# Optimization experiments

Hardware: AMD Instinct MI355X
Metric: run time of the kernel (lower is better)

Reference implementation:

```python
import jax, jax.numpy as jnp
import numpy as np

DIM = 768
H = 12
D = DIM // H            # 64
SCALE = D ** -0.5
M = 64                  # landmarks for pnp heads
PINV_ITERS = 6
PNP_HEADS = 11          # heads 0..10 use Nystrom, head 11 uses softmax


def setup_inputs() -> dict:
    key = jax.random.key(0)
    ks = jax.random.split(key, 5)
    B, N = 4, 4096
    x = jax.random.normal(ks[0], (B, N, DIM), jnp.float32)
    qkv_w = jax.random.normal(ks[1], (3 * DIM, DIM), jnp.float32) * (DIM ** -0.5)
    qkv_b = jax.random.normal(ks[2], (3 * DIM,), jnp.float32) * 0.01
    proj_w = jax.random.normal(ks[3], (DIM, DIM), jnp.float32) * (DIM ** -0.5)
    proj_b = jax.random.normal(ks[4], (DIM,), jnp.float32) * 0.01
    return {"x": x, "qkv_w": qkv_w, "qkv_b": qkv_b, "proj_w": proj_w, "proj_b": proj_b}


def moore_penrose_iter_pinv(x, iters=PINV_ITERS):
    # x: [B, h, M, M]. Original torch code takes torch.max over the whole per-head
    # tensor (incl. batch), so normalize with a per-head scalar over axes (B, M).
    abs_x = jnp.abs(x)
    col_max = abs_x.sum(axis=-1, keepdims=True).max(axis=(0, 2, 3), keepdims=True)
    row_max = abs_x.sum(axis=-2, keepdims=True).max(axis=(0, 2, 3), keepdims=True)
    z = jnp.swapaxes(x, -1, -2) / (col_max * row_max)
    I = jnp.eye(x.shape[-1], dtype=x.dtype)
    for _ in range(iters):
        xz = x @ z
        z = 0.25 * (z @ (13.0 * I - xz @ (15.0 * I - xz @ (7.0 * I - xz))))
    return z


def reference(x, qkv_w, qkv_b, proj_w, proj_b):
    B, N, C = x.shape
    qkv = (x @ qkv_w.T + qkv_b).reshape(B, N, 3, H, D).transpose(2, 0, 3, 1, 4)  # [3,B,H,N,D]
    q, k, v = qkv[0] * SCALE, qkv[1], qkv[2]

    # ---- Nystrom (pnp) heads 0..PNP_HEADS-1, all with the same M -> vectorized ----
    qp, kp, vp = q[:, :PNP_HEADS], k[:, :PNP_HEADS], v[:, :PNP_HEADS]
    idxs = jnp.array([int(i * N / M) for i in range(M)], dtype=jnp.int32)
    q_m = qp[:, :, idxs, :]   # [B,h,M,D] landmark queries
    k_m = kp[:, :, idxs, :]   # [B,h,M,D] landmark keys

    SA = jnp.einsum('bhnd,bhmd->bhnm', qp, k_m)   # [B,h,N,M]
    SC = jnp.einsum('bhmd,bhnd->bhmn', q_m, kp)   # [B,h,M,N]
    SB = jnp.einsum('bhmd,bhld->bhml', q_m, k_m)  # [B,h,M,M]

    eA = jnp.exp(SA - SA.max(axis=-1, keepdims=True))
    sc_max = SC.max(axis=-1, keepdims=True)       # [B,h,M,1]
    eC = jnp.exp(SC - sc_max)
    eB = jnp.exp(jnp.clip(SB - sc_max, -88.0, None))

    v_aug = jnp.concatenate([vp, jnp.ones_like(vp[..., :1])], axis=-1)  # [B,h,N,D+1]
    pi = moore_penrose_iter_pinv(eB)
    prod = (eA @ pi) @ (eC @ v_aug)               # [B,h,N,D+1]
    out_p = prod[..., :-1] / jnp.maximum(prod[..., -1:], 1e-8)

    # ---- fallback softmax head(s) ----
    qs, ks_, vs = q[:, PNP_HEADS:], k[:, PNP_HEADS:], v[:, PNP_HEADS:]
    attn = jax.nn.softmax(jnp.einsum('bhnd,bhmd->bhnm', qs, ks_), axis=-1)
    out_s = attn @ vs

    ctx = jnp.concatenate([out_p, out_s], axis=1).transpose(0, 2, 1, 3).reshape(B, N, C)
    return ctx @ proj_w.T + proj_b
```

## Files before the change

kernel.cpp:

```cpp
#include <hip/hip_runtime.h>


typedef __attribute__((ext_vector_type(8))) short short8;
typedef __attribute__((ext_vector_type(4))) float f32x4;
typedef __attribute__((ext_vector_type(4))) unsigned short ushort4v;

static __device__ __forceinline__ unsigned short f2bf(float f) {
    union { float f; unsigned u; } x; x.f = f;
    unsigned r = x.u + 0x7fffu + ((x.u >> 16) & 1u);
    return (unsigned short)(r >> 16);
}

static __device__ __forceinline__ float b2f(unsigned short u) {
    union { unsigned u; float f; } t; t.u = (unsigned)u << 16; return t.f;
}

static __device__ __forceinline__ void bfsplit(float x, unsigned short& h, unsigned short& l) {
    unsigned short hh = f2bf(x);
    union { unsigned u; float f; } t; t.u = (unsigned)hh << 16;
    h = hh;
    l = f2bf(x - t.f);
}

__global__ __launch_bounds__(256) void preconv3(
    const float* __restrict__ a, const float* __restrict__ b,
    const float* __restrict__ c,
    unsigned short* __restrict__ ahi, unsigned short* __restrict__ alo,
    unsigned short* __restrict__ bhi, unsigned short* __restrict__ blo,
    unsigned short* __restrict__ chi, unsigned short* __restrict__ clo)
{
    const int nA = 3145728, nB = 442368, nC = 147456;
    const int total = nA + nB + nC;
    for (int i = blockIdx.x * 256 + threadIdx.x; i < total; i += gridDim.x * 256) {
        const float* src; unsigned short* hi; unsigned short* lo; int j;
        if (i < nA)           { src = a; hi = ahi; lo = alo; j = i; }
        else if (i < nA + nB) { src = b; hi = bhi; lo = blo; j = i - nA; }
        else                  { src = c; hi = chi; lo = clo; j = i - nA - nB; }
        float4 f = *(const float4*)(src + (size_t)j * 4);
        float vs[4] = {f.x, f.y, f.z, f.w};
        ushort4v h, l;
        #pragma unroll
        for (int t = 0; t < 4; ++t) {
            unsigned short hh, ll;
            bfsplit(vs[t], hh, ll);
            h[t] = hh; l[t] = ll;
        }
        *(ushort4v*)(hi + (size_t)j * 4) = h;
        *(ushort4v*)(lo + (size_t)j * 4) = l;
    }
}

__global__ __launch_bounds__(256, 2) void gemm_qkv2(
    const unsigned short* __restrict__ Xh, const unsigned short* __restrict__ Xl,
    const unsigned short* __restrict__ Wh, const unsigned short* __restrict__ Wl,
    const float* __restrict__ bias,
    unsigned short* __restrict__ qh, unsigned short* __restrict__ ql,
    unsigned short* __restrict__ kh, unsigned short* __restrict__ kl,
    unsigned short* __restrict__ vh)
{
    __shared__ unsigned short smem[16384];
    const int tid = threadIdx.x;
    const int ln = tid & 63, wv = tid >> 6;
    const int wr = (wv >> 1) << 6, wc = (wv & 1) << 6;
    const int fr = ln & 15, fc = ln >> 4;
    const int fg = ln >> 4;

    if (blockIdx.x < 1536) {
        unsigned short* Ah = smem;
        unsigned short* Al = smem + 4096;
        unsigned short* Bh = smem + 8192;
        unsigned short* Bl = smem + 12288;
        const int bid = blockIdx.x;
        const int swz = (bid & 7) * 192 + (bid >> 3);
        const int brow = (swz / 12) << 7, bcol = (swz % 12) << 7;
        const int srow = tid >> 1, sc = (tid & 1) << 1;
        const size_t ag = (size_t)(brow + srow) * 768 + (sc << 3);
        const size_t bg = (size_t)(bcol + srow) * 768 + (sc << 3);
        const int i0 = srow * 32 + (((sc + 0) ^ (srow & 3)) << 3);
        const int i1 = srow * 32 + (((sc + 1) ^ (srow & 3)) << 3);

        f32x4 acc[4][4] = {};
        for (int k0 = 0; k0 < 768; k0 += 32) {
            short8 xh0 = *(const short8*)(Xh + ag + k0);
            short8 xh1 = *(const short8*)(Xh + ag + k0 + 8);
            short8 xl0 = *(const short8*)(Xl + ag + k0);
            short8 xl1 = *(const short8*)(Xl + ag + k0 + 8);
            short8 wh0 = *(const short8*)(Wh + bg + k0);
            short8 wh1 = *(const short8*)(Wh + bg + k0 + 8);
            short8 wl0 = *(const short8*)(Wl + bg + k0);
            short8 wl1 = *(const short8*)(Wl + bg + k0 + 8);
            __syncthreads();
            *(short8*)&Ah[i0] = xh0; *(short8*)&Ah[i1] = xh1;
            *(short8*)&Al[i0] = xl0; *(short8*)&Al[i1] = xl1;
            *(short8*)&Bh[i0] = wh0; *(short8*)&Bh[i1] = wh1;
            *(short8*)&Bl[i0] = wl0; *(short8*)&Bl[i1] = wl1;
            __syncthreads();
            short8 ah[4], al[4], bh[4], bl[4];
            #pragma unroll
            for (int i = 0; i < 4; ++i) {
                int ar = wr + (i << 4) + fr;
                int aidx = ar * 32 + ((fc ^ (ar & 3)) << 3);
                ah[i] = *(short8*)&Ah[aidx];
                al[i] = *(short8*)&Al[aidx];
                int br2 = wc + (i << 4) + fr;
                int bidx = br2 * 32 + ((fc ^ (br2 & 3)) << 3);
                bh[i] = *(short8*)&Bh[bidx];
                bl[i] = *(short8*)&Bl[bidx];
            }
            #pragma unroll
            for (int i = 0; i < 4; ++i)
                #pragma unroll
                for (int j = 0; j < 4; ++j) {
                    acc[i][j] = __builtin_amdgcn_mfma_f32_16x16x32_bf16(ah[i], bh[j], acc[i][j], 0, 0, 0);
                    acc[i][j] = __builtin_amdgcn_mfma_f32_16x16x32_bf16(ah[i], bl[j], acc[i][j], 0, 0, 0);
                    acc[i][j] = __builtin_amdgcn_mfma_f32_16x16x32_bf16(al[i], bh[j], acc[i][j], 0, 0, 0);
                }
        }
        #pragma unroll
        for (int j = 0; j < 4; ++j) {
            int c = bcol + wc + (j << 4) + fr;
            float bb = bias[c];
            int rem = c - (c >= 768 ? 768 : 0);
            int h = rem >> 6, d = rem & 63;
            #pragma unroll
            for (int i = 0; i < 4; ++i)
                #pragma unroll
                for (int r = 0; r < 4; ++r) {
                    int row = brow + wr + (i << 4) + (fg << 2) + r;
                    int b = row >> 12, n = row & 4095;
                    float val = acc[i][j][r] + bb;
                    size_t idx = (((size_t)(b * 12 + h) << 12) + n) * 64 + d;
                    unsigned short hh, ll;
                    if (c < 768) {
                        bfsplit(val * 0.125f, hh, ll);
                        qh[idx] = hh; ql[idx] = ll;
                    } else {
                        bfsplit(val, hh, ll);
                        kh[idx] = hh; kl[idx] = ll;
                    }
                }
        }
    } else {
        unsigned short* Av = smem;
        unsigned short* Bv = smem + 8192;
        const int bid = blockIdx.x - 1536;
        const int swz = (bid & 7) * 96 + (bid >> 3);
        const int brow = (swz / 6) << 7, bcol = 1536 + ((swz % 6) << 7);
        const int srow = tid >> 1;
        const int c0 = (tid & 1) << 2;
        const size_t ag = (size_t)(brow + srow) * 768;
        const size_t bg = (size_t)(bcol + srow) * 768;

        f32x4 acc[4][4] = {};
        for (int k0 = 0; k0 < 768; k0 += 64) {
            short8 xa[4], wb[4];
            #pragma unroll
            for (int cc = 0; cc < 4; ++cc) {
                xa[cc] = *(const short8*)(Xh + ag + k0 + ((c0 + cc) << 3));
                wb[cc] = *(const short8*)(Wh + bg + k0 + ((c0 + cc) << 3));
            }
            __syncthreads();
            #pragma unroll
            for (int cc = 0; cc < 4; ++cc) {
                int dst = srow * 64 + (((c0 + cc) ^ (srow & 7)) << 3);
                *(short8*)&Av[dst] = xa[cc];
                *(short8*)&Bv[dst] = wb[cc];
            }
            __syncthreads();
            #pragma unroll
            for (int ks = 0; ks < 2; ++ks) {
                const int kc = (ks << 2) + fc;
                short8 ah[4], bh[4];
                #pragma unroll
                for (int i = 0; i < 4; ++i) {
                    int ar = wr + (i << 4) + fr;
                    ah[i] = *(short8*)&Av[ar * 64 + ((kc ^ (ar & 7)) << 3)];
                    int br2 = wc + (i << 4) + fr;
                    bh[i] = *(short8*)&Bv[br2 * 64 + ((kc ^ (br2 & 7)) << 3)];
                }
                #pragma unroll
                for (int i = 0; i < 4; ++i)
                    #pragma unroll
                    for (int j = 0; j < 4; ++j)
                        acc[i][j] = __builtin_amdgcn_mfma_f32_16x16x32_bf16(ah[i], bh[j], acc[i][j], 0, 0, 0);
            }
        }
        #pragma unroll
        for (int j = 0; j < 4; ++j) {
            int c = bcol + wc + (j << 4) + fr;
            float bb = bias[c];
            int rem = c - 1536;
            int h = rem >> 6, d = rem & 63;
            #pragma unroll
            for (int i = 0; i < 4; ++i)
                #pragma unroll
                for (int r = 0; r < 4; ++r) {
                    int row = brow + wr + (i << 4) + (fg << 2) + r;
                    int b = row >> 12, n = row & 4095;
                    float val = acc[i][j][r] + bb;
                    size_t idx = (((size_t)(b * 12 + h) << 12) + n) * 64 + d;
                    vh[idx] = f2bf(val);
                }
        }
    }
}

__global__ __launch_bounds__(256) void attn_mega(
    const unsigned short* __restrict__ qh, const unsigned short* __restrict__ ql,
    const unsigned short* __restrict__ khg, const unsigned short* __restrict__ klg,
    const unsigned short* __restrict__ vhg,
    float* __restrict__ wacc, float* __restrict__ wl, float* __restrict__ wm,
    float* __restrict__ pacc, float* __restrict__ pm, float* __restrict__ pl)
{
    __shared__ unsigned short kh_s[64][72], kl_s[64][72];
    __shared__ unsigned short vth[64][72];
    __shared__ unsigned short ph[4][16][72];
    int tid = threadIdx.x;
    int wv = tid >> 6, ln = tid & 63;
    int rr = tid >> 2, dg = (tid & 3) << 4;
    const int arow = (wv << 4) + (ln & 15);
    const int ak0 = (ln >> 4) << 3;
    const int rg = (ln >> 4) << 2;

    if (blockIdx.x < 1024) {
        int fbid = blockIdx.x;
        int bx = fbid & 63, cy = (fbid >> 6) & 3, b = fbid >> 8;
        int n0 = bx << 6;
        size_t base = ((size_t)(b * 12 + 11)) << 12;
        {
            size_t off = ((base + n0 + rr) << 6) + dg;
            *(short8*)&kh_s[rr][dg]     = *(const short8*)(qh + off);
            *(short8*)&kh_s[rr][dg + 8] = *(const short8*)(qh + off + 8);
        }
        __syncthreads();
        short8 aq0 = *(short8*)&kh_s[arow][ak0];
        short8 aq1 = *(short8*)&kh_s[arow][ak0 + 32];
        f32x4 o_acc[4] = {};
        float mr[4] = {-1e30f, -1e30f, -1e30f, -1e30f};
        float lr[4] = {};
        for (int t = 0; t < 16; ++t) {
            int m0 = (cy << 10) + (t << 6);
            __syncthreads();
            {
                size_t off = ((base + m0 + rr) << 6) + dg;
                *(short8*)&kl_s[rr][dg]     = *(const short8*)(khg + off);
                *(short8*)&kl_s[rr][dg + 8] = *(const short8*)(khg + off + 8);
                short8 v0 = *(const short8*)(vhg + off);
                short8 v1 = *(const short8*)(vhg + off + 8);
                #pragma unroll
                for (int i = 0; i < 8; ++i) {
                    vth[dg + i][rr]     = (unsigned short)v0[i];
                    vth[dg + 8 + i][rr] = (unsigned short)v1[i];
                }
            }
            __syncthreads();
            f32x4 s_acc[4];
            #pragma unroll
            for (int jb = 0; jb < 4; ++jb) {
                f32x4 z = {};
                short8 bk0 = *(short8*)&kl_s[(jb << 4) + (ln & 15)][ak0];
                short8 bk1 = *(short8*)&kl_s[(jb << 4) + (ln & 15)][ak0 + 32];
                z = __builtin_amdgcn_mfma_f32_16x16x32_bf16(aq0, bk0, z, 0, 0, 0);
                z = __builtin_amdgcn_mfma_f32_16x16x32_bf16(aq1, bk1, z, 0, 0, 0);
                s_acc[jb] = z;
            }
            float mx[4];
            #pragma unroll
            for (int r = 0; r < 4; ++r)
                mx[r] = fmaxf(fmaxf(s_acc[0][r], s_acc[1][r]),
                              fmaxf(s_acc[2][r], s_acc[3][r]));
            #pragma unroll
            for (int off2 = 1; off2 < 16; off2 <<= 1)
                #pragma unroll
                for (int r = 0; r < 4; ++r)
                    mx[r] = fmaxf(mx[r], __shfl_xor(mx[r], off2, 64));
            float fac[4];
            #pragma unroll
            for (int r = 0; r < 4; ++r) {
                float mn = fmaxf(mr[r], mx[r]);
                fac[r] = expf(mr[r] - mn);
                mr[r] = mn;
            }
            float rs[4] = {};
            #pragma unroll
            for (int jb = 0; jb < 4; ++jb)
                #pragma unroll
                for (int r = 0; r < 4; ++r) {
                    float p = expf(s_acc[jb][r] - mr[r]);
                    rs[r] += p;
                    ph[wv][rg + r][(jb << 4) + (ln & 15)] = f2bf(p);
                }
            #pragma unroll
            for (int off2 = 1; off2 < 16; off2 <<= 1)
                #pragma unroll
                for (int r = 0; r < 4; ++r)
                    rs[r] += __shfl_xor(rs[r], off2, 64);
            #pragma unroll
            for (int r = 0; r < 4; ++r) lr[r] = lr[r] * fac[r] + rs[r];
            #pragma unroll
            for (int jb = 0; jb < 4; ++jb)
                #pragma unroll
                for (int r = 0; r < 4; ++r)
                    o_acc[jb][r] *= fac[r];
            short8 pa0 = *(short8*)&ph[wv][ln & 15][ak0];
            short8 pa1 = *(short8*)&ph[wv][ln & 15][ak0 + 32];
            #pragma unroll
            for (int jb = 0; jb < 4; ++jb) {
                short8 bv0 = *(short8*)&vth[(jb << 4) + (ln & 15)][ak0];
                short8 bv1 = *(short8*)&vth[(jb << 4) + (ln & 15)][ak0 + 32];
                f32x4 z = o_acc[jb];
                z = __builtin_amdgcn_mfma_f32_16x16x32_bf16(pa0, bv0, z, 0, 0, 0);
                z = __builtin_amdgcn_mfma_f32_16x16x32_bf16(pa1, bv1, z, 0, 0, 0);
                o_acc[jb] = z;
            }
        }
        int slot = (b * 4 + cy) * 64 + bx;
        #pragma unroll
        for (int jb = 0; jb < 4; ++jb)
            #pragma unroll
            for (int r = 0; r < 4; ++r) {
                int row = (wv << 4) + rg + r, col = (jb << 4) + (ln & 15);
                pacc[(size_t)slot * 4096 + (size_t)row * 64 + col] = o_acc[jb][r];
            }
        if ((ln & 15) == 0)
            #pragma unroll
            for (int r = 0; r < 4; ++r) {
                int row = (wv << 4) + rg + r;
                pm[(size_t)slot * 64 + row] = mr[r];
                pl[(size_t)slot * 64 + row] = lr[r];
            }
    } else {
        int wbid = blockIdx.x - 1024;
        int chunk = wbid & 7;
        int bh = wbid >> 3;
        int b = bh / 11, h = bh - b * 11;
        size_t base = ((size_t)(b * 12 + h)) << 12;
        short8 aqh0, aql0, aqh1, aql1;
        {
            size_t off = ((base + ((size_t)arow << 6)) << 6) + ak0;
            aqh0 = *(const short8*)(qh + off);
            aqh1 = *(const short8*)(qh + off + 32);
            aql0 = *(const short8*)(ql + off);
            aql1 = *(const short8*)(ql + off + 32);
        }
        f32x4 o_acc[4] = {};
        float mr[4] = {-1e30f, -1e30f, -1e30f, -1e30f};
        float lr[4] = {};
        for (int t = 0; t < 8; ++t) {
            int n0 = (chunk << 9) + (t << 6);
            __syncthreads();
            {
                size_t off = ((base + n0 + rr) << 6) + dg;
                *(short8*)&kh_s[rr][dg]     = *(const short8*)(khg + off);
                *(short8*)&kh_s[rr][dg + 8] = *(const short8*)(khg + off + 8);
                *(short8*)&kl_s[rr][dg]     = *(const short8*)(klg + off);
                *(short8*)&kl_s[rr][dg + 8] = *(const short8*)(klg + off + 8);
                short8 v0 = *(const short8*)(vhg + off);
                short8 v1 = *(const short8*)(vhg + off + 8);
                #pragma unroll
                for (int i = 0; i < 8; ++i) {
                    vth[dg + i][rr]     = (unsigned short)v0[i];
                    vth[dg + 8 + i][rr] = (unsigned short)v1[i];
                }
            }
            __syncthreads();
            f32x4 s_acc[4];
            #pragma unroll
            for (int jb = 0; jb < 4; ++jb) {
                f32x4 z = {};
                const int brow2 = (jb << 4) + (ln & 15);
                short8 bh0 = *(short8*)&kh_s[brow2][ak0];
                short8 bh1 = *(short8*)&kh_s[brow2][ak0 + 32];
                short8 bl0 = *(short8*)&kl_s[brow2][ak0];
                short8 bl1 = *(short8*)&kl_s[brow2][ak0 + 32];
                z = __builtin_amdgcn_mfma_f32_16x16x32_bf16(aqh0, bh0, z, 0, 0, 0);
                z = __builtin_amdgcn_mfma_f32_16x16x32_bf16(aqh0, bl0, z, 0, 0, 0);
                z = __builtin_amdgcn_mfma_f32_16x16x32_bf16(aql0, bh0, z, 0, 0, 0);
                z = __builtin_amdgcn_mfma_f32_16x16x32_bf16(aqh1, bh1, z, 0, 0, 0);
                z = __builtin_amdgcn_mfma_f32_16x16x32_bf16(aqh1, bl1, z, 0, 0, 0);
                z = __builtin_amdgcn_mfma_f32_16x16x32_bf16(aql1, bh1, z, 0, 0, 0);
                s_acc[jb] = z;
            }
            float mx[4];
            #pragma unroll
            for (int r = 0; r < 4; ++r)
                mx[r] = fmaxf(fmaxf(s_acc[0][r], s_acc[1][r]),
                              fmaxf(s_acc[2][r], s_acc[3][r]));
            #pragma unroll
            for (int off2 = 1; off2 < 16; off2 <<= 1)
                #pragma unroll
                for (int r = 0; r < 4; ++r)
                    mx[r] = fmaxf(mx[r], __shfl_xor(mx[r], off2, 64));
            float fac[4];
            #pragma unroll
            for (int r = 0; r < 4; ++r) {
                float mn = fmaxf(mr[r], mx[r]);
                fac[r] = expf(mr[r] - mn);
                mr[r] = mn;
            }
            float rs[4] = {};
            #pragma unroll
            for (int jb = 0; jb < 4; ++jb)
                #pragma unroll
                for (int r = 0; r < 4; ++r) {
                    float p = expf(s_acc[jb][r] - mr[r]);
                    rs[r] += p;
                    ph[wv][rg + r][(jb << 4) + (ln & 15)] = f2bf(p);
                }
            #pragma unroll
            for (int off2 = 1; off2 < 16; off2 <<= 1)
                #pragma unroll
                for (int r = 0; r < 4; ++r)
                    rs[r] += __shfl_xor(rs[r], off2, 64);
            #pragma unroll
            for (int r = 0; r < 4; ++r) lr[r] = lr[r] * fac[r] + rs[r];
            #pragma unroll
            for (int jb = 0; jb < 4; ++jb)
                #pragma unroll
                for (int r = 0; r < 4; ++r)
                    o_acc[jb][r] *= fac[r];
            short8 pah0 = *(short8*)&ph[wv][ln & 15][ak0];
            short8 pah1 = *(short8*)&ph[wv][ln & 15][ak0 + 32];
            #pragma unroll
            for (int jb = 0; jb < 4; ++jb) {
                const int brow2 = (jb << 4) + (ln & 15);
                short8 bv0 = *(short8*)&vth[brow2][ak0];
                short8 bv1 = *(short8*)&vth[brow2][ak0 + 32];
                f32x4 o = o_acc[jb];
                o = __builtin_amdgcn_mfma_f32_16x16x32_bf16(pah0, bv0, o, 0, 0, 0);
                o = __builtin_amdgcn_mfma_f32_16x16x32_bf16(pah1, bv1, o, 0, 0, 0);
                o_acc[jb] = o;
            }
        }
        int cidx = (bh << 3) + chunk;
        #pragma unroll
        for (int jb = 0; jb < 4; ++jb)
            #pragma unroll
            for (int r = 0; r < 4; ++r) {
                int row = (wv << 4) + rg + r, col = (jb << 4) + (ln & 15);
                wacc[((size_t)cidx << 12) + ((size_t)row << 6) + col] = o_acc[jb][r];
            }
        if ((ln & 15) == 0)
            #pragma unroll
            for (int r = 0; r < 4; ++r) {
                int row = (wv << 4) + rg + r;
                wl[cidx * 64 + row] = lr[r];
                wm[cidx * 64 + row] = mr[r];
            }
    }
}

__global__ __launch_bounds__(256) void wmerge_eb(
    const float* __restrict__ wacc, const float* __restrict__ wl,
    const float* __restrict__ wm,
    const unsigned short* __restrict__ qh, const unsigned short* __restrict__ ql,
    const unsigned short* __restrict__ kh, const unsigned short* __restrict__ kl,
    float* __restrict__ Wb, float* __restrict__ eB)
{
    int bh = blockIdx.x;
    int b = bh / 11, h = bh - b * 11;
    size_t base = ((size_t)(b * 12 + h)) << 12;
    int tid = threadIdx.x;
    __shared__ float fcs[8][64];
    __shared__ float scms[64];
    __shared__ float qm[64][65], km[64][65];
    for (int e = tid; e < 4096; e += 256) {
        int mm = e >> 6, d = e & 63;
        size_t off = ((base + ((size_t)mm << 6)) << 6) + d;
        qm[mm][d] = b2f(qh[off]) + b2f(ql[off]);
        km[mm][d] = b2f(kh[off]) + b2f(kl[off]);
    }
    if (tid < 64) {
        float mx = -1e30f;
        #pragma unroll
        for (int c = 0; c < 8; ++c)
            mx = fmaxf(mx, wm[((bh << 3) + c) * 64 + tid]);
        scms[tid] = mx;
        #pragma unroll
        for (int c = 0; c < 8; ++c)
            fcs[c][tid] = expf(wm[((bh << 3) + c) * 64 + tid] - mx);
    }
    __syncthreads();
    for (int e = tid; e < 4096; e += 256) {
        int m = e >> 6, j = e & 63;
        float s = 0.f;
        #pragma unroll
        for (int c = 0; c < 8; ++c)
            s += fcs[c][m] * wacc[((size_t)((bh << 3) + c) << 12) + e];
        Wb[(size_t)bh * 4160 + m * 65 + j] = s;
    }
    if (tid < 64) {
        float s = 0.f;
        #pragma unroll
        for (int c = 0; c < 8; ++c)
            s += fcs[c][tid] * wl[((bh << 3) + c) * 64 + tid];
        Wb[(size_t)bh * 4160 + tid * 65 + 64] = s;
    }
    int m = tid >> 2, l0 = tid & 3;
    float smax = scms[m];
    for (int l = l0; l < 64; l += 4) {
        float s = 0.f;
        #pragma unroll
        for (int d = 0; d < 64; ++d) s += qm[m][d] * km[l][d];
        eB[((size_t)bh << 12) + (m << 6) + l] = expf(fmaxf(s - smax, -88.f));
    }
}

__global__ __launch_bounds__(256) void norms_kernel(
    const float* __restrict__ eB, float* __restrict__ denom)
{
    int h = blockIdx.x;
    int tid = threadIdx.x;
    int b = tid >> 6, idx = tid & 63;
    int bh = b * 11 + h;
    const float* E = eB + ((size_t)bh << 12);
    float rs = 0.f, cs = 0.f;
    #pragma unroll 4
    for (int l = 0; l < 64; ++l) rs += E[(idx << 6) + l];
    #pragma unroll 4
    for (int m = 0; m < 64; ++m) cs += E[(m << 6) + idx];
    __shared__ float r1[256], r2[256];
    r1[tid] = rs; r2[tid] = cs;
    __syncthreads();
    for (int s = 128; s > 0; s >>= 1) {
        if (tid < s) {
            r1[tid] = fmaxf(r1[tid], r1[tid + s]);
            r2[tid] = fmaxf(r2[tid], r2[tid + s]);
        }
        __syncthreads();
    }
    if (tid == 0) denom[h] = r1[0] * r2[0];
}

__device__ __forceinline__ void mm64x3(
    const unsigned short (&Ahi)[64][72], const unsigned short (&Alo)[64][72],
    const unsigned short (&BThi)[64][72], const unsigned short (&BTlo)[64][72],
    int wr, int wc, int fr, int fk, f32x4 (&acc)[2][2])
{
    #pragma unroll
    for (int ks = 0; ks < 2; ++ks) {
        const int kb = (ks << 5) + fk;
        short8 ah[2], al[2], bh[2], bl[2];
        #pragma unroll
        for (int i = 0; i < 2; ++i) {
            ah[i] = *(const short8*)&Ahi[wr + (i << 4) + fr][kb];
            al[i] = *(const short8*)&Alo[wr + (i << 4) + fr][kb];
            bh[i] = *(const short8*)&BThi[wc + (i << 4) + fr][kb];
            bl[i] = *(const short8*)&BTlo[wc + (i << 4) + fr][kb];
        }
        #pragma unroll
        for (int i = 0; i < 2; ++i)
            #pragma unroll
            for (int j = 0; j < 2; ++j) {
                acc[i][j] = __builtin_amdgcn_mfma_f32_16x16x32_bf16(ah[i], bh[j], acc[i][j], 0, 0, 0);
                acc[i][j] = __builtin_amdgcn_mfma_f32_16x16x32_bf16(ah[i], bl[j], acc[i][j], 0, 0, 0);
                acc[i][j] = __builtin_amdgcn_mfma_f32_16x16x32_bf16(al[i], bh[j], acc[i][j], 0, 0, 0);
            }
    }
}

__global__ __launch_bounds__(256) void pinv_kernel(
    const float* __restrict__ eB, const float* __restrict__ denom,
    float* __restrict__ pi_)
{
    __shared__ unsigned short Xh[64][72],  Xl[64][72];
    __shared__ unsigned short Zh[64][72],  Zl[64][72];
    __shared__ unsigned short ZTh[64][72], ZTl[64][72];
    __shared__ unsigned short Mh[64][72],  Ml[64][72];
    __shared__ unsigned short MTh[64][72], MTl[64][72];
    __shared__ unsigned short Th[64][72],  Tbl[64][72];
    __shared__ float Zf[64][68];
    int bh = blockIdx.x;
    int h = bh % 11;
    int tid = threadIdx.x;
    float dn = denom[h];
    const int ln = tid & 63, wv = tid >> 6;
    const int wr = (wv >> 1) << 5, wc = (wv & 1) << 5;
    const int fr = ln & 15, fk = (ln >> 4) << 3;
    const int rg = (ln >> 4) << 2;

    for (int e = tid; e < 4096; e += 256) {
        int m = e >> 6, l = e & 63;
        float xv = eB[((size_t)bh << 12) + e];
        unsigned short hh, ll;
        bfsplit(xv, hh, ll);
        Xh[m][l] = hh; Xl[m][l] = ll;
        float zv = xv / dn;
        Zf[l][m] = zv;
        bfsplit(zv, hh, ll);
        Zh[l][m] = hh; Zl[l][m] = ll;
        ZTh[m][l] = hh; ZTl[m][l] = ll;
    }
    __syncthreads();

    for (int it = 0; it < 6; ++it) {
        f32x4 mm1[2][2] = {};
        mm64x3(Xh, Xl, ZTh, ZTl, wr, wc, fr, fk, mm1);
        #pragma unroll
        for (int i = 0; i < 2; ++i)
            #pragma unroll
            for (int j = 0; j < 2; ++j)
                #pragma unroll
                for (int r = 0; r < 4; ++r) {
                    int row = wr + (i << 4) + rg + r, col = wc + (j << 4) + fr;
                    unsigned short hh, ll;
                    bfsplit(mm1[i][j][r], hh, ll);
                    Mh[row][col] = hh;  Ml[row][col] = ll;
                    MTh[col][row] = hh; MTl[col][row] = ll;
                }
        __syncthreads();
        f32x4 a2[2][2] = {};
        mm64x3(Mh, Ml, MTh, MTl, wr, wc, fr, fk, a2);
        #pragma unroll
        for (int i = 0; i < 2; ++i)
            #pragma unroll
            for (int j = 0; j < 2; ++j)
                #pragma unroll
                for (int r = 0; r < 4; ++r) {
                    int row = wr + (i << 4) + rg + r, col = wc + (j << 4) + fr;
                    float val = 7.f * mm1[i][j][r] - a2[i][j][r];
                    unsigned short hh, ll;
                    bfsplit(val, hh, ll);
                    Th[col][row] = hh; Tbl[col][row] = ll;
                }
        __syncthreads();
        f32x4 a3[2][2] = {};
        mm64x3(Mh, Ml, Th, Tbl, wr, wc, fr, fk, a3);
        __syncthreads();
        #pragma unroll
        for (int i = 0; i < 2; ++i)
            #pragma unroll
            for (int j = 0; j < 2; ++j)
                #pragma unroll
                for (int r = 0; r < 4; ++r) {
                    int row = wr + (i << 4) + rg + r, col = wc + (j << 4) + fr;
                    float val = 15.f * mm1[i][j][r] - a3[i][j][r];
                    unsigned short hh, ll;
                    bfsplit(val, hh, ll);
                    Th[col][row] = hh; Tbl[col][row] = ll;
                }
        __syncthreads();
        f32x4 a4[2][2] = {};
        mm64x3(Zh, Zl, Th, Tbl, wr, wc, fr, fk, a4);
        float zn[2][2][4];
        #pragma unroll
        for (int i = 0; i < 2; ++i)
            #pragma unroll
            for (int j = 0; j < 2; ++j)
                #pragma unroll
                for (int r = 0; r < 4; ++r) {
                    int row = wr + (i << 4) + rg + r, col = wc + (j << 4) + fr;
                    zn[i][j][r] = 0.25f * (13.f * Zf[row][col] - a4[i][j][r]);
                }
        __syncthreads();
        #pragma unroll
        for (int i = 0; i < 2; ++i)
            #pragma unroll
            for (int j = 0; j < 2; ++j)
                #pragma unroll
                for (int r = 0; r < 4; ++r) {
                    int row = wr + (i << 4) + rg + r, col = wc + (j << 4) + fr;
                    float val = zn[i][j][r];
                    Zf[row][col] = val;
                    unsigned short hh, ll;
                    bfsplit(val, hh, ll);
                    Zh[row][col] = hh;  Zl[row][col] = ll;
                    ZTh[col][row] = hh; ZTl[col][row] = ll;
                }
        __syncthreads();
    }
    for (int e = tid; e < 4096; e += 256)
        pi_[((size_t)bh << 12) + e] = Zf[e >> 6][e & 63];
}

__global__ __launch_bounds__(256) void pw_kernel(
    const float* __restrict__ pi_, const float* __restrict__ Wb,
    float* __restrict__ Tb)
{
    int bh = blockIdx.x;
    __shared__ float P[64][65];
    __shared__ float Wl[64][66];
    int tid = threadIdx.x;
    for (int e = tid; e < 4096; e += 256)
        P[e >> 6][e & 63] = pi_[((size_t)bh << 12) + e];
    for (int e = tid; e < 64 * 65; e += 256) {
        int l = e / 65, j = e - l * 65;
        Wl[l][j] = Wb[(size_t)bh * 4160 + e];
    }
    __syncthreads();
    int m = tid & 63, g = tid >> 6;
    #pragma unroll
    for (int t = 0; t < 17; ++t) {
        int j = g + (t << 2);
        if (j > 64) break;
        float s = 0.f;
        #pragma unroll
        for (int l = 0; l < 64; ++l) s += P[m][l] * Wl[l][j];
        Tb[(size_t)((bh << 6) + m) * 65 + j] = s;
    }
}

__global__ __launch_bounds__(256) void outp_merge(
    const unsigned short* __restrict__ qh, const unsigned short* __restrict__ ql,
    const unsigned short* __restrict__ khg, const unsigned short* __restrict__ klg,
    const float* __restrict__ Tb,
    const float* __restrict__ pacc, const float* __restrict__ pm,
    const float* __restrict__ pl,
    unsigned short* __restrict__ ctxh)
{
    int tid = threadIdx.x;
    if (blockIdx.x < 2816) {
        int bh = blockIdx.x >> 6;
        int bx = blockIdx.x & 63;
        int b = bh / 11, h = bh - b * 11;
        int n0 = bx << 6;
        size_t base = ((size_t)(b * 12 + h)) << 12;
        __shared__ unsigned short kmh[64][72], kml[64][72];
        __shared__ unsigned short tth[64][72], ttl[64][72];
        __shared__ unsigned short ph[4][16][72];
        __shared__ float t64[64];
        int wv = tid >> 6, ln = tid & 63;
        int rr = tid >> 2, dg = (tid & 3) << 4;
        const int arow = (wv << 4) + (ln & 15);
        const int ak0 = (ln >> 4) << 3;
        const int rg = (ln >> 4) << 2;
        {
            size_t off = ((base + ((size_t)rr << 6)) << 6) + dg;
            *(short8*)&kmh[rr][dg]     = *(const short8*)(khg + off);
            *(short8*)&kmh[rr][dg + 8] = *(const short8*)(khg + off + 8);
            *(short8*)&kml[rr][dg]     = *(const short8*)(klg + off);
            *(short8*)&kml[rr][dg + 8] = *(const short8*)(klg + off + 8);
        }
        for (int e = tid; e < 4096; e += 256) {
            int m = e >> 6, j = e & 63;
            float tv = Tb[(size_t)((bh << 6) + m) * 65 + j];
            unsigned short hh, ll;
            bfsplit(tv, hh, ll);
            tth[j][m] = hh; ttl[j][m] = ll;
        }
        if (tid < 64) t64[tid] = Tb[(size_t)((bh << 6) + tid) * 65 + 64];
        short8 aqh0, aql0, aqh1, aql1;
        {
            size_t off = ((base + n0 + arow) << 6) + ak0;
            aqh0 = *(const short8*)(qh + off);
            aqh1 = *(const short8*)(qh + off + 32);
            aql0 = *(const short8*)(ql + off);
            aql1 = *(const short8*)(ql + off + 32);
        }
        __syncthreads();
        f32x4 s_acc[4];
        #pragma unroll
        for (int jb = 0; jb < 4; ++jb) {
            f32x4 z = {};
            const int brow2 = (jb << 4) + (ln & 15);
            short8 bh0 = *(short8*)&kmh[brow2][ak0];
            short8 bh1 = *(short8*)&kmh[brow2][ak0 + 32];
            short8 bl0 = *(short8*)&kml[brow2][ak0];
            short8 bl1 = *(short8*)&kml[brow2][ak0 + 32];
            z = __builtin_amdgcn_mfma_f32_16x16x32_bf16(aqh0, bh0, z, 0, 0, 0);
            z = __builtin_amdgcn_mfma_f32_16x16x32_bf16(aqh0, bl0, z, 0, 0, 0);
            z = __builtin_amdgcn_mfma_f32_16x16x32_bf16(aql0, bh0, z, 0, 0, 0);
            z = __builtin_amdgcn_mfma_f32_16x16x32_bf16(aqh1, bh1, z, 0, 0, 0);
            z = __builtin_amdgcn_mfma_f32_16x16x32_bf16(aqh1, bl1, z, 0, 0, 0);
            z = __builtin_amdgcn_mfma_f32_16x16x32_bf16(aql1, bh1, z, 0, 0, 0);
            s_acc[jb] = z;
        }
        float mx[4];
        #pragma unroll
        for (int r = 0; r < 4; ++r)
            mx[r] = fmaxf(fmaxf(s_acc[0][r], s_acc[1][r]),
                          fmaxf(s_acc[2][r], s_acc[3][r]));
        #pragma unroll
        for (int off2 = 1; off2 < 16; off2 <<= 1)
            #pragma unroll
            for (int r = 0; r < 4; ++r)
                mx[r] = fmaxf(mx[r], __shfl_xor(mx[r], off2, 64));
        float den[4] = {};
        #pragma unroll
        for (int jb = 0; jb < 4; ++jb) {
            float tj = t64[(jb << 4) + (ln & 15)];
            #pragma unroll
            for (int r = 0; r < 4; ++r) {
                float p = expf(s_acc[jb][r] - mx[r]);
                den[r] += p * tj;
                ph[wv][rg + r][(jb << 4) + (ln & 15)] = f2bf(p);
            }
        }
        #pragma unroll
        for (int off2 = 1; off2 < 16; off2 <<= 1)
            #pragma unroll
            for (int r = 0; r < 4; ++r)
                den[r] += __shfl_xor(den[r], off2, 64);
        short8 pah0 = *(short8*)&ph[wv][ln & 15][ak0];
        short8 pah1 = *(short8*)&ph[wv][ln & 15][ak0 + 32];
        f32x4 o_acc[4] = {};
        #pragma unroll
        for (int jb = 0; jb < 4; ++jb) {
            const int brow2 = (jb << 4) + (ln & 15);
            short8 bth0 = *(short8*)&tth[brow2][ak0];
            short8 bth1 = *(short8*)&tth[brow2][ak0 + 32];
            short8 btl0 = *(short8*)&ttl[brow2][ak0];
            short8 btl1 = *(short8*)&ttl[brow2][ak0 + 32];
            f32x4 o = o_acc[jb];
            o = __builtin_amdgcn_mfma_f32_16x16x32_bf16(pah0, bth0, o, 0, 0, 0);
            o = __builtin_amdgcn_mfma_f32_16x16x32_bf16(pah0, btl0, o, 0, 0, 0);
            o = __builtin_amdgcn_mfma_f32_16x16x32_bf16(pah1, bth1, o, 0, 0, 0);
            o = __builtin_amdgcn_mfma_f32_16x16x32_bf16(pah1, btl1, o, 0, 0, 0);
            o_acc[jb] = o;
        }
        float inv[4];
        #pragma unroll
        for (int r = 0; r < 4; ++r) inv[r] = 1.0f / fmaxf(den[r], 1e-8f);
        #pragma unroll
        for (int jb = 0; jb < 4; ++jb)
            #pragma unroll
            for (int r = 0; r < 4; ++r) {
                int row = n0 + (wv << 4) + rg + r;
                int col = (jb << 4) + (ln & 15);
                ctxh[((size_t)b * 4096 + row) * 768 + h * 64 + col] =
                    f2bf(o_acc[jb][r] * inv[r]);
            }
    } else {
        int fb = blockIdx.x - 2816;
        int bx = fb & 63, b = fb >> 6;
        int r = tid & 63, g = tid >> 6;
        float mc[4], mt = -1e30f;
        #pragma unroll
        for (int c = 0; c < 4; ++c) {
            mc[c] = pm[(size_t)((b * 4 + c) * 64 + bx) * 64 + r];
            mt = fmaxf(mt, mc[c]);
        }
        float fac[4], lt = 0.f;
        #pragma unroll
        for (int c = 0; c < 4; ++c) {
            fac[c] = expf(mc[c] - mt);
            lt += fac[c] * pl[(size_t)((b * 4 + c) * 64 + bx) * 64 + r];
        }
        float inv = 1.0f / lt;
        size_t obase = ((size_t)b * 4096 + (size_t)((bx << 6) + r)) * 768 + 11 * 64 + (g << 4);
        #pragma unroll
        for (int i = 0; i < 16; ++i) {
            float s = 0.f;
            #pragma unroll
            for (int c = 0; c < 4; ++c)
                s += fac[c] * pacc[(size_t)((b * 4 + c) * 64 + bx) * 4096 + (size_t)r * 64 + (g << 4) + i];
            ctxh[obase + i] = f2bf(s * inv);
        }
    }
}

__global__ __launch_bounds__(256, 2) void gemm_proj_mfma(
    const unsigned short* __restrict__ Xh, const unsigned short* __restrict__ Wh,
    const float* __restrict__ bias, float* __restrict__ out)
{
    __shared__ unsigned short Ah[8192], Bh[8192];
    const int tid = threadIdx.x;
    const int bid = blockIdx.x;
    const int swz = (bid & 7) * 96 + (bid >> 3);
    const int brow = (swz / 6) << 7, bcol = (swz % 6) << 7;
    const int ln = tid & 63, wv = tid >> 6;
    const int wr = (wv >> 1) << 6, wc = (wv & 1) << 6;
    const int srow = tid >> 1;
    const int c0 = (tid & 1) << 2;
    const size_t ag = (size_t)(brow + srow) * 768;
    const size_t bg = (size_t)(bcol + srow) * 768;
    const int fr = ln & 15, fc = ln >> 4;

    f32x4 acc[4][4] = {};
    for (int k0 = 0; k0 < 768; k0 += 64) {
        short8 xa[4], wb[4];
        #pragma unroll
        for (int cc = 0; cc < 4; ++cc) {
            xa[cc] = *(const short8*)(Xh + ag + k0 + ((c0 + cc) << 3));
            wb[cc] = *(const short8*)(Wh + bg + k0 + ((c0 + cc) << 3));
        }
        __syncthreads();
        #pragma unroll
        for (int cc = 0; cc < 4; ++cc) {
            int dst = srow * 64 + (((c0 + cc) ^ (srow & 7)) << 3);
            *(short8*)&Ah[dst] = xa[cc];
            *(short8*)&Bh[dst] = wb[cc];
        }
        __syncthreads();
        #pragma unroll
        for (int ks = 0; ks < 2; ++ks) {
            const int kc = (ks << 2) + fc;
            short8 ah[4], bh[4];
            #pragma unroll
            for (int i = 0; i < 4; ++i) {
                int ar = wr + (i << 4) + fr;
                ah[i] = *(short8*)&Ah[ar * 64 + ((kc ^ (ar & 7)) << 3)];
                int br2 = wc + (i << 4) + fr;
                bh[i] = *(short8*)&Bh[br2 * 64 + ((kc ^ (br2 & 7)) << 3)];
            }
            #pragma unroll
            for (int i = 0; i < 4; ++i)
                #pragma unroll
                for (int j = 0; j < 4; ++j)
                    acc[i][j] = __builtin_amdgcn_mfma_f32_16x16x32_bf16(ah[i], bh[j], acc[i][j], 0, 0, 0);
        }
    }
    const int fg = ln >> 4;
    #pragma unroll
    for (int j = 0; j < 4; ++j) {
        int c = bcol + wc + (j << 4) + fr;
        float bb = bias[c];
        #pragma unroll
        for (int i = 0; i < 4; ++i)
            #pragma unroll
            for (int r = 0; r < 4; ++r) {
                int row = brow + wr + (i << 4) + (fg << 2) + r;
                out[(size_t)row * 768 + c] = acc[i][j][r] + bb;
            }
    }
}

extern "C" void kernel_launch(void* const* d_in, const int* in_sizes, int n_in,
                              void* d_out, int out_size, void* d_ws, size_t ws_size,
                              hipStream_t stream)
{
    const float* x      = (const float*)d_in[0];
    const float* qkv_w  = (const float*)d_in[1];
    const float* qkv_b  = (const float*)d_in[2];
    const float* proj_w = (const float*)d_in[3];
    const float* proj_b = (const float*)d_in[4];
    float* out = (float*)d_out;

    const size_t QKV = (size_t)4 * 12 * 4096 * 64;
    unsigned short* qh = (unsigned short*)d_ws;
    unsigned short* ql = qh + QKV;
    unsigned short* kh = ql + QKV;
    unsigned short* kl = kh + QKV;
    unsigned short* vh = kl + QKV;
    unsigned short* ctxh = vh + QKV;
    float* eB   = (float*)(ctxh + QKV);
    float* den  = eB + 44 * 4096;
    float* pi_  = den + 64;
    float* Wb   = pi_ + 44 * 4096;
    float* Tb   = Wb + 44 * 4160;
    unsigned short* Whi  = (unsigned short*)(Tb + 44 * 4160);
    unsigned short* Wlo  = Whi + (size_t)2304 * 768;
    unsigned short* Pwhi = Wlo + (size_t)2304 * 768;
    unsigned short* Pwlo = Pwhi + (size_t)768 * 768;

    unsigned short* Xhi = (unsigned short*)out;
    unsigned short* Xlo = Xhi + QKV;
    float* wacc  = out;
    float* wl    = wacc + 1441792;
    float* wm    = wl + 22528;
    float* fpacc = wm + 22528;
    float* fpm   = fpacc + 4194304;
    float* fpl   = fpm + 65536;

    preconv3<<<2048, 256, 0, stream>>>(x, qkv_w, proj_w,
                                       Xhi, Xlo, Whi, Wlo, Pwhi, Pwlo);
    gemm_qkv2<<<2304, 256, 0, stream>>>(Xhi, Xlo, Whi, Wlo, qkv_b,
                                        qh, ql, kh, kl, vh);
    attn_mega<<<1376, 256, 0, stream>>>(qh, ql, kh, kl, vh,
                                        wacc, wl, wm, fpacc, fpm, fpl);
    wmerge_eb<<<44, 256, 0, stream>>>(wacc, wl, wm, qh, ql, kh, kl, Wb, eB);
    norms_kernel<<<11, 256, 0, stream>>>(eB, den);
    pinv_kernel<<<44, 256, 0, stream>>>(eB, den, pi_);
    pw_kernel<<<44, 256, 0, stream>>>(pi_, Wb, Tb);
    outp_merge<<<3072, 256, 0, stream>>>(qh, ql, kh, kl, Tb,
                                         fpacc, fpm, fpl, ctxh);
    gemm_proj_mfma<<<768, 256, 0, stream>>>(ctxh, Pwhi, proj_b, out);
}
```

Baseline: 409.5 us.

## Fuse norm reduction into wmerge and pw product into pinv kernel

Per-head row/column sum maxima for the pinv normalisation are now computed inside wmerge_eb from a shared-memory copy of eB. They are combined across batches with float atomicMax into buffers zeroed by a memset, which removes the separate norms_kernel launch. The pi@Wb product now runs at the end of the pinv kernel straight from the Zf shared tile, so the pi_ round trip through global memory and the pw_kernel launch go away. This cuts two small launches but adds a memset, atomics and extra shared memory in both kernels.

```diff
diff --git a/kernel.cpp b/kernel.cpp
--- a/kernel.cpp
+++ b/kernel.cpp
@@ -455,7 +455,8 @@
     const float* __restrict__ wm,
     const unsigned short* __restrict__ qh, const unsigned short* __restrict__ ql,
     const unsigned short* __restrict__ kh, const unsigned short* __restrict__ kl,
-    float* __restrict__ Wb, float* __restrict__ eB)
+    float* __restrict__ Wb, float* __restrict__ eB,
+    float* __restrict__ denr, float* __restrict__ denc)
 {
     int bh = blockIdx.x;
     int b = bh / 11, h = bh - b * 11;
@@ -464,6 +465,7 @@
     __shared__ float fcs[8][64];
     __shared__ float scms[64];
     __shared__ float qm[64][65], km[64][65];
+    __shared__ float ebs[64][65];
     for (int e = tid; e < 4096; e += 256) {
         int mm = e >> 6, d = e & 63;
         size_t off = ((base + ((size_t)mm << 6)) << 6) + d;
@@ -502,34 +504,28 @@
         float s = 0.f;
         #pragma unroll
         for (int d = 0; d < 64; ++d) s += qm[m][d] * km[l][d];
-        eB[((size_t)bh << 12) + (m << 6) + l] = expf(fmaxf(s - smax, -88.f));
-    }
-}
-
-__global__ __launch_bounds__(256) void norms_kernel(
-    const float* __restrict__ eB, float* __restrict__ denom)
-{
-    int h = blockIdx.x;
-    int tid = threadIdx.x;
-    int b = tid >> 6, idx = tid & 63;
-    int bh = b * 11 + h;
-    const float* E = eB + ((size_t)bh << 12);
-    float rs = 0.f, cs = 0.f;
-    #pragma unroll 4
-    for (int l = 0; l < 64; ++l) rs += E[(idx << 6) + l];
-    #pragma unroll 4
-    for (int m = 0; m < 64; ++m) cs += E[(m << 6) + idx];
-    __shared__ float r1[256], r2[256];
-    r1[tid] = rs; r2[tid] = cs;
+        float ev = expf(fmaxf(s - smax, -88.f));
+        eB[((size_t)bh << 12) + (m << 6) + l] = ev;
+        ebs[m][l] = ev;
+    }
     __syncthreads();
-    for (int s = 128; s > 0; s >>= 1) {
-        if (tid < s) {
-            r1[tid] = fmaxf(r1[tid], r1[tid + s]);
-            r2[tid] = fmaxf(r2[tid], r2[tid + s]);
-        }
-        __syncthreads();
-    }
-    if (tid == 0) denom[h] = r1[0] * r2[0];
+    if (tid < 64) {
+        float rs = 0.f, cs = 0.f;
+        #pragma unroll 4
+        for (int l = 0; l < 64; ++l) rs += ebs[tid][l];
+        #pragma unroll 4
+        for (int mm = 0; mm < 64; ++mm) cs += ebs[mm][tid];
+        float rmax = rs, cmax = cs;
+        #pragma unroll
+        for (int off = 1; off < 64; off <<= 1) {
+            rmax = fmaxf(rmax, __shfl_xor(rmax, off, 64));
+            cmax = fmaxf(cmax, __shfl_xor(cmax, off, 64));
+        }
+        if (tid == 0) {
+            atomicMax((unsigned*)&denr[h], __float_as_uint(rmax));
+            atomicMax((unsigned*)&denc[h], __float_as_uint(cmax));
+        }
+    }
 }
 
 __device__ __forceinline__ void mm64x3(
@@ -559,9 +555,10 @@
     }
 }
 
-__global__ __launch_bounds__(256) void pinv_kernel(
-    const float* __restrict__ eB, const float* __restrict__ denom,
-    float* __restrict__ pi_)
+__global__ __launch_bounds__(256) void pinv_pw(
+    const float* __restrict__ eB,
+    const float* __restrict__ denr, const float* __restrict__ denc,
+    const float* __restrict__ Wb, float* __restrict__ Tb)
 {
     __shared__ unsigned short Xh[64][72],  Xl[64][72];
     __shared__ unsigned short Zh[64][72],  Zl[64][72];
@@ -569,16 +566,21 @@
     __shared__ unsigned short Mh[64][72],  Ml[64][72];
     __shared__ unsigned short MTh[64][72], MTl[64][72];
     __shared__ unsigned short Th[64][72],  Tbl[64][72];
-    __shared__ float Zf[64][68];
+    __shared__ float Zf[64][69];
+    __shared__ float Wls[64][66];
     int bh = blockIdx.x;
     int h = bh % 11;
     int tid = threadIdx.x;
-    float dn = denom[h];
+    float dn = denr[h] * denc[h];
     const int ln = tid & 63, wv = tid >> 6;
     const int wr = (wv >> 1) << 5, wc = (wv & 1) << 5;
     const int fr = ln & 15, fk = (ln >> 4) << 3;
     const int rg = (ln >> 4) << 2;
 
+    for (int e = tid; e < 4160; e += 256) {
+        int l = e / 65, j = e - l * 65;
+        Wls[l][j] = Wb[(size_t)bh * 4160 + e];
+    }
     for (int e = tid; e < 4096; e += 256) {
         int m = e >> 6, l = e & 63;
         float xv = eB[((size_t)bh << 12) + e];
@@ -669,34 +671,15 @@
                 }
         __syncthreads();
     }
-    for (int e = tid; e < 4096; e += 256)
-        pi_[((size_t)bh << 12) + e] = Zf[e >> 6][e & 63];
-}
-
-__global__ __launch_bounds__(256) void pw_kernel(
-    const float* __restrict__ pi_, const float* __restrict__ Wb,
-    float* __restrict__ Tb)
-{
-    int bh = blockIdx.x;
-    __shared__ float P[64][65];
-    __shared__ float Wl[64][66];
-    int tid = threadIdx.x;
-    for (int e = tid; e < 4096; e += 256)
-        P[e >> 6][e & 63] = pi_[((size_t)bh << 12) + e];
-    for (int e = tid; e < 64 * 65; e += 256) {
-        int l = e / 65, j = e - l * 65;
-        Wl[l][j] = Wb[(size_t)bh * 4160 + e];
-    }
-    __syncthreads();
-    int m = tid & 63, g = tid >> 6;
+    int m2 = tid & 63, g2 = tid >> 6;
     #pragma unroll
     for (int t = 0; t < 17; ++t) {
-        int j = g + (t << 2);
+        int j = g2 + (t << 2);
         if (j > 64) break;
         float s = 0.f;
         #pragma unroll
-        for (int l = 0; l < 64; ++l) s += P[m][l] * Wl[l][j];
-        Tb[(size_t)((bh << 6) + m) * 65 + j] = s;
+        for (int l = 0; l < 64; ++l) s += Zf[m2][l] * Wls[l][j];
+        Tb[(size_t)((bh << 6) + m2) * 65 + j] = s;
     }
 }
 
@@ -934,9 +917,9 @@
     unsigned short* vh = kl + QKV;
     unsigned short* ctxh = vh + QKV;
     float* eB   = (float*)(ctxh + QKV);
-    float* den  = eB + 44 * 4096;
-    float* pi_  = den + 64;
-    float* Wb   = pi_ + 44 * 4096;
+    float* denr = eB + 44 * 4096;
+    float* denc = denr + 16;
+    float* Wb   = denc + 16;
     float* Tb   = Wb + 44 * 4160;
     unsigned short* Whi  = (unsigned short*)(Tb + 44 * 4160);
     unsigned short* Wlo  = Whi + (size_t)2304 * 768;
@@ -952,16 +935,16 @@
     float* fpm   = fpacc + 4194304;
     float* fpl   = fpm + 65536;
 
+    hipMemsetAsync(denr, 0, 32 * sizeof(float), stream);
     preconv3<<<2048, 256, 0, stream>>>(x, qkv_w, proj_w,
                                        Xhi, Xlo, Whi, Wlo, Pwhi, Pwlo);
     gemm_qkv2<<<2304, 256, 0, stream>>>(Xhi, Xlo, Whi, Wlo, qkv_b,
                                         qh, ql, kh, kl, vh);
     attn_mega<<<1376, 256, 0, stream>>>(qh, ql, kh, kl, vh,
                                         wacc, wl, wm, fpacc, fpm, fpl);
-    wmerge_eb<<<44, 256, 0, stream>>>(wacc, wl, wm, qh, ql, kh, kl, Wb, eB);
-    norms_kernel<<<11, 256, 0, stream>>>(eB, den);
-    pinv_kernel<<<44, 256, 0, stream>>>(eB, den, pi_);
-    pw_kernel<<<44, 256, 0, stream>>>(pi_, Wb, Tb);
+    wmerge_eb<<<44, 256, 0, stream>>>(wacc, wl, wm, qh, ql, kh, kl,
+                                      Wb, eB, denr, denc);
+    pinv_pw<<<44, 256, 0, stream>>>(eB, denr, denc, Wb, Tb);
     outp_merge<<<3072, 256, 0, stream>>>(qh, ql, kh, kl, Tb,
                                          fpacc, fpm, fpl, ctxh);
     gemm_proj_mfma<<<768, 256, 0, stream>>>(ctxh, Pwhi, proj_b, out);
```

Result: no change. 407.8 us (-0.4%).
